# Kernel tuning notes

Hardware: AMD Instinct MI355X
Metric: run time of the kernel (lower is better)

Reference implementation:

```python
import jax, jax.numpy as jnp
import numpy as np

EMBED_DIM = 64
NUM_HEADS = 8
D_K = EMBED_DIM // NUM_HEADS  # 8
B, S = 8, 1024


def setup_inputs() -> dict:
    key = jax.random.key(0)
    ks = jax.random.split(key, 10)
    f32 = jnp.float32
    lim = 1.0 / np.sqrt(EMBED_DIM)
    def lin(k):
        kw, kb = jax.random.split(k)
        w = jax.random.uniform(kw, (EMBED_DIM, EMBED_DIM), f32, -lim, lim)
        b = jax.random.uniform(kb, (EMBED_DIM,), f32, -lim, lim)
        return w, b
    wq, bq = lin(ks[0])
    wk, bk = lin(ks[1])
    wv, bv = lin(ks[2])
    wo, bo = lin(ks[3])
    theta = jax.random.normal(ks[4], (EMBED_DIM,), f32)  # trainable RY angles, one per wire
    x = jax.random.normal(ks[5], (B, S, EMBED_DIM), f32)
    return {"x": x, "wq": wq, "bq": bq, "wk": wk, "bk": bk,
            "wv": wv, "bv": bv, "theta": theta, "wo": wo, "bo": bo}


def _quantum_map(t, theta):
    # Per-qubit circuit on |0>: RX(t_i) encode, RY(theta_i), <PauliZ_i>.
    # Product state => <Z_i> = cos(theta_i) * cos(t_i) exactly.
    return jnp.cos(theta) * jnp.cos(t.reshape(-1, EMBED_DIM))  # [N, E]


def reference(x, wq, bq, wk, bk, wv, bv, theta, wo, bo):
    # Linear QKV (torch nn.Linear: x @ W^T + b)
    q = x @ wq.T + bq
    k = x @ wk.T + bk
    v = x @ wv.T + bv
    # Quantum measurement map, flattened over batch*seq (as in the original)
    q_q = _quantum_map(q, theta)  # [N, E], N = B*S
    k_q = _quantum_map(k, theta)
    v_q = _quantum_map(v, theta)
    # Full flattened attention: [N, N] scores (original never reshapes back)
    scores = (q_q @ k_q.T) / jnp.sqrt(jnp.asarray(D_K, x.dtype))
    attn = jax.nn.softmax(scores, axis=-1)  # dropout is identity in eval
    out = attn @ v_q  # [N, E]
    return out @ wo.T + bo
```

## Files before the change

kernel.cpp:

```cpp
#include <hip/hip_runtime.h>
#include <hip/hip_bf16.h>

#define NQ 8192
#define DIM 64
#define SPLITS 16
#define FQB 64
#define KEYS_PER_SPLIT (NQ / SPLITS)
#define NSTEPS (KEYS_PER_SPLIT / 32)
#define GRID_FLASH ((NQ / FQB) * SPLITS)
#define MERGEB 1024
#define MROWS (NQ / MERGEB)
#define SC2 0.51012301920911057f
#define KSTR 72

typedef short s8v __attribute__((ext_vector_type(8)));
typedef short s4v __attribute__((ext_vector_type(4)));
typedef float f4v __attribute__((ext_vector_type(4)));
typedef int   i4v __attribute__((ext_vector_type(4)));

__device__ __forceinline__ float b2f(short s) {
  unsigned int u = ((unsigned int)(unsigned short)s) << 16;
  return __uint_as_float(u);
}
__device__ __forceinline__ float b2f_lo(unsigned int u) {
  return __uint_as_float(u << 16);
}
__device__ __forceinline__ float b2f_hi(unsigned int u) {
  return __uint_as_float(u & 0xffff0000u);
}
__device__ __forceinline__ short f2b(float f) {
  __hip_bfloat16 h = __float2bfloat16(f);
  return *reinterpret_cast<short*>(&h);
}
__device__ __forceinline__ int pack_bf16x2(float a, float b) {
  union { __hip_bfloat162 h; int i; } u;
  u.h = __float22bfloat162_rn(make_float2(a, b));
  return u.i;
}
__device__ __forceinline__ float fast_exp2(float x) {
#if __has_builtin(__builtin_amdgcn_exp2f)
  return __builtin_amdgcn_exp2f(x);
#else
  return exp2f(x);
#endif
}

__global__ __launch_bounds__(64) void qkv_kernel(
    const float* __restrict__ x,
    const float* __restrict__ wq, const float* __restrict__ bq,
    const float* __restrict__ wk, const float* __restrict__ bk,
    const float* __restrict__ wv, const float* __restrict__ bv,
    const float* __restrict__ theta,
    short* __restrict__ qq, short* __restrict__ kvT) {
  int lane = threadIdx.x & 63;
  int l15 = lane & 15, quad = lane >> 4;
  int tg = blockIdx.x;
  int mg = blockIdx.y;
  int n = tg * 16 + l15;

  const float* W  = (mg == 0) ? wq : (mg == 1) ? wk : wv;
  const float* Bb = (mg == 0) ? bq : (mg == 1) ? bk : bv;

  const float* xr = x + (size_t)n * DIM + quad * 8;
  float4 x0 = *(const float4*)&xr[0];
  float4 x1 = *(const float4*)&xr[4];
  float4 x2 = *(const float4*)&xr[32];
  float4 x3 = *(const float4*)&xr[36];
  s8v xf0 = {f2b(x0.x), f2b(x0.y), f2b(x0.z), f2b(x0.w),
             f2b(x1.x), f2b(x1.y), f2b(x1.z), f2b(x1.w)};
  s8v xf1 = {f2b(x2.x), f2b(x2.y), f2b(x2.z), f2b(x2.w),
             f2b(x3.x), f2b(x3.y), f2b(x3.z), f2b(x3.w)};

  size_t tb = (size_t)(n >> 6) * 8192;
  int nperm = (n & 3) | ((n & 16) >> 2);
  size_t vbase = tb + 4096 + ((n & 32) >> 5) * 2048 + ((n & 15) >> 2) * 128 + nperm;

#pragma unroll
  for (int i = 0; i < 4; ++i) {
    const float* wr = W + (size_t)(i * 16 + l15) * DIM + quad * 8;
    float4 a0 = *(const float4*)&wr[0];
    float4 a1 = *(const float4*)&wr[4];
    float4 a2 = *(const float4*)&wr[32];
    float4 a3 = *(const float4*)&wr[36];
    s8v wf0 = {f2b(a0.x), f2b(a0.y), f2b(a0.z), f2b(a0.w),
               f2b(a1.x), f2b(a1.y), f2b(a1.z), f2b(a1.w)};
    s8v wf1 = {f2b(a2.x), f2b(a2.y), f2b(a2.z), f2b(a2.w),
               f2b(a3.x), f2b(a3.y), f2b(a3.z), f2b(a3.w)};
    f4v acc = (f4v){0.f, 0.f, 0.f, 0.f};
    acc = __builtin_amdgcn_mfma_f32_16x16x32_bf16(wf0, xf0, acc, 0, 0, 0);
    acc = __builtin_amdgcn_mfma_f32_16x16x32_bf16(wf1, xf1, acc, 0, 0, 0);
    int d0 = i * 16 + quad * 4;
    float4 bias = *(const float4*)&Bb[d0];
    float4 th4 = *(const float4*)&theta[d0];
    float y0 = __cosf(acc[0] + bias.x) * __cosf(th4.x);
    float y1 = __cosf(acc[1] + bias.y) * __cosf(th4.y);
    float y2 = __cosf(acc[2] + bias.z) * __cosf(th4.z);
    float y3 = __cosf(acc[3] + bias.w) * __cosf(th4.w);
    if (mg == 0) {
      s4v p = {f2b(SC2 * y0), f2b(SC2 * y1), f2b(SC2 * y2), f2b(SC2 * y3)};
      *(s4v*)&qq[(size_t)n * DIM + d0] = p;
    } else if (mg == 1) {
      int e = d0;
      size_t idx = tb + ((n & 63) >> 4) * 1024 + (e >> 5) * 512 +
                   ((e & 31) >> 3) * 128 + (n & 15) * 8 + (e & 7);
      s4v p = {f2b(y0), f2b(y1), f2b(y2), f2b(y3)};
      *(s4v*)&kvT[idx] = p;
    } else {
      float ys[4] = {y0, y1, y2, y3};
#pragma unroll
      for (int r = 0; r < 4; ++r) {
        int e = d0 + r;
        kvT[vbase + (e >> 4) * 512 + (e & 15) * 8] = f2b(ys[r]);
      }
    }
  }
}

#if __has_builtin(__builtin_amdgcn_global_load_lds)
#define DMA_CHUNK(srcp, dstp) \
  __builtin_amdgcn_global_load_lds( \
      (const __attribute__((address_space(1))) void*)(srcp), \
      (__attribute__((address_space(3))) void*)(dstp), 16, 0, 0)
#else
#define DMA_CHUNK(srcp, dstp) \
  { *(s8v*)((short*)(dstp) + (threadIdx.x & 63) * 8) = \
        *(const s8v*)((const short*)(srcp)); }
#endif

__global__ __launch_bounds__(64, 2) void flash_kernel(
    const short* __restrict__ qq, const short* __restrict__ kvT,
    short* __restrict__ pO, short* __restrict__ pL) {
  __shared__ __align__(16) short lds[2][4096];

  int lane = threadIdx.x & 63;
  int l15 = lane & 15, quad = lane >> 4;
  int qblock = blockIdx.x >> 4, split = blockIdx.x & 15;
  int qbase = qblock * FQB;

  s8v qf[4][2];
#pragma unroll
  for (int qt = 0; qt < 4; ++qt) {
    const short* qr = qq + (qbase + qt * 16 + l15) * DIM + quad * 8;
    qf[qt][0] = *(const s8v*)qr;
    qf[qt][1] = *(const s8v*)(qr + 32);
  }
  asm volatile("s_waitcnt vmcnt(0)" ::: "memory");

  const short ONE = (short)0x3F80;
  const s8v ones = {ONE, ONE, ONE, ONE, ONE, ONE, ONE, ONE};

  f4v o[4][4], ol[4];
#pragma unroll
  for (int qt = 0; qt < 4; ++qt) {
    ol[qt] = (f4v){0.f, 0.f, 0.f, 0.f};
#pragma unroll
    for (int c = 0; c < 4; ++c) o[qt][c] = (f4v){0.f, 0.f, 0.f, 0.f};
  }

  const short* kvs = kvT + (size_t)(split * (KEYS_PER_SPLIT / 64)) * 8192 +
                     lane * 8;
#define STAGE32(S, BUF)                                                      \
  {                                                                          \
    const short* s_ = kvs + ((S) >> 1) * 8192 + ((S) & 1) * 2048;            \
    short* d_ = &lds[BUF][0];                                                \
    _Pragma("unroll") for (int c2 = 0; c2 < 4; ++c2) {                       \
      DMA_CHUNK(s_ + c2 * 512, d_ + c2 * 512);                               \
      DMA_CHUNK(s_ + 4096 + c2 * 512, d_ + 2048 + c2 * 512);                 \
    }                                                                        \
  }

  STAGE32(0, 0)

  for (int s = 0; s < NSTEPS; ++s) {
    if (s + 1 < NSTEPS) {
      STAGE32(s + 1, (s + 1) & 1)
      asm volatile("s_waitcnt vmcnt(8)" ::: "memory");
    } else {
      asm volatile("s_waitcnt vmcnt(0)" ::: "memory");
    }
    __builtin_amdgcn_sched_barrier(0);

    const short* kb = lds[s & 1];
    const short* vb = kb + 2048;

    i4v pai[4];
#pragma unroll
    for (int h = 0; h < 2; ++h) {
      s8v kf0 = *(const s8v*)&kb[(h * 2) * 512 + lane * 8];
      s8v kf1 = *(const s8v*)&kb[(h * 2 + 1) * 512 + lane * 8];
#pragma unroll
      for (int qt = 0; qt < 4; ++qt) {
        f4v acc = (f4v){0.f, 0.f, 0.f, 0.f};
        acc = __builtin_amdgcn_mfma_f32_16x16x32_bf16(kf0, qf[qt][0], acc, 0, 0, 0);
        acc = __builtin_amdgcn_mfma_f32_16x16x32_bf16(kf1, qf[qt][1], acc, 0, 0, 0);
        pai[qt][h * 2]     = pack_bf16x2(fast_exp2(acc[0]), fast_exp2(acc[1]));
        pai[qt][h * 2 + 1] = pack_bf16x2(fast_exp2(acc[2]), fast_exp2(acc[3]));
      }
    }
    __builtin_amdgcn_s_setprio(1);
#pragma unroll
    for (int qt = 0; qt < 4; ++qt)
      ol[qt] = __builtin_amdgcn_mfma_f32_16x16x32_bf16(
          __builtin_bit_cast(s8v, pai[qt]), ones, ol[qt], 0, 0, 0);
#pragma unroll
    for (int c = 0; c < 4; ++c) {
      s8v vf = *(const s8v*)&vb[c * 512 + lane * 8];
#pragma unroll
      for (int qt = 0; qt < 4; ++qt)
        o[qt][c] = __builtin_amdgcn_mfma_f32_16x16x32_bf16(
            __builtin_bit_cast(s8v, pai[qt]), vf, o[qt][c], 0, 0, 0);
    }
    __builtin_amdgcn_s_setprio(0);
  }

#pragma unroll
  for (int qt = 0; qt < 4; ++qt) {
#pragma unroll
    for (int r = 0; r < 4; ++r) {
      int q = qbase + qt * 16 + quad * 4 + r;
      short* dst = pO + ((size_t)split * NQ + q) * DIM;
#pragma unroll
      for (int c = 0; c < 4; ++c) dst[c * 16 + l15] = f2b(o[qt][c][r]);
      if (l15 == 0) pL[(size_t)split * NQ + q] = f2b(ol[qt][r]);
    }
  }
}

__global__ __launch_bounds__(256) void merge_kernel(
    const short* __restrict__ pO, const short* __restrict__ pL,
    const float* __restrict__ wo, const float* __restrict__ bo,
    float* __restrict__ out) {
  __shared__ __align__(16) short wsh[DIM * KSTR];
  __shared__ __align__(16) float att[MROWS * DIM];
  int tid = threadIdx.x;
  int q0 = blockIdx.x * MROWS;
  for (int i = tid; i < DIM * 16; i += 256) {
    int r = i >> 4, c4 = (i & 15) << 2;
    float4 w = *(const float4*)&wo[r * DIM + c4];
    s4v p = {f2b(w.x), f2b(w.y), f2b(w.z), f2b(w.w)};
    *(s4v*)&wsh[r * KSTR + c4] = p;
  }
  {
    int e2 = (tid & 31) * 2, rg8 = tid >> 5;
    int q = q0 + rg8;
    const short* psrc = pO + (size_t)q * DIM + e2;
    const short* lsrc = pL + q;
    float a0 = 0.f, a1 = 0.f, l = 0.f;
#pragma unroll
    for (int sp = 0; sp < SPLITS; ++sp) {
      unsigned int u = *(const unsigned int*)&psrc[(size_t)sp * NQ * DIM];
      a0 += b2f_lo(u);
      a1 += b2f_hi(u);
      l += b2f(lsrc[(size_t)sp * NQ]);
    }
#if __has_builtin(__builtin_amdgcn_rcpf)
    float ri = __builtin_amdgcn_rcpf(l);
#else
    float ri = 1.f / l;
#endif
    att[rg8 * DIM + e2] = a0 * ri;
    att[rg8 * DIM + e2 + 1] = a1 * ri;
  }
  __syncthreads();
  int e = tid & 63, rg = tid >> 6;
  for (int rr = rg; rr < MROWS; rr += 4) {
    float acc = bo[e];
#pragma unroll
    for (int c8 = 0; c8 < 8; ++c8) {
      s8v w = *(const s8v*)&wsh[e * KSTR + c8 * 8];
      const float* ar = &att[rr * DIM + c8 * 8];
      acc += ar[0] * b2f(w[0]) + ar[1] * b2f(w[1]) + ar[2] * b2f(w[2]) + ar[3] * b2f(w[3])
           + ar[4] * b2f(w[4]) + ar[5] * b2f(w[5]) + ar[6] * b2f(w[6]) + ar[7] * b2f(w[7]);
    }
    out[(size_t)(q0 + rr) * DIM + e] = acc;
  }
}

extern "C" void kernel_launch(void* const* d_in, const int* in_sizes, int n_in,
                              void* d_out, int out_size, void* d_ws, size_t ws_size,
                              hipStream_t stream) {
  const float* x  = (const float*)d_in[0];
  const float* wq = (const float*)d_in[1];
  const float* bq = (const float*)d_in[2];
  const float* wk = (const float*)d_in[3];
  const float* bk = (const float*)d_in[4];
  const float* wv = (const float*)d_in[5];
  const float* bv = (const float*)d_in[6];
  const float* th = (const float*)d_in[7];
  const float* wo = (const float*)d_in[8];
  const float* bo = (const float*)d_in[9];

  char* ws = (char*)d_ws;
  short* qq  = (short*)(ws);
  short* kvT = (short*)(ws + (1u << 20));
  short* pO  = (short*)(ws + (3u << 20));
  short* pL  = (short*)(ws + (19u << 20));

  hipLaunchKernelGGL(qkv_kernel, dim3(NQ / 16, 3), dim3(64), 0, stream,
                     x, wq, bq, wk, bk, wv, bv, th, qq, kvT);
  hipLaunchKernelGGL(flash_kernel, dim3(GRID_FLASH), dim3(FQB), 0, stream,
                     qq, kvT, pO, pL);
  hipLaunchKernelGGL(merge_kernel, dim3(MERGEB), dim3(256), 0, stream,
                     pO, pL, wo, bo, (float*)d_out);
}
```

Measured before the change: 113.6 us.

## Fuse split merge and output projection into flash kernel via last-block atomic counter

Removes the separate merge kernel. Each flash block atomically increments a per-query-block counter, and the last split to finish reduces the partial outputs and row sums, then applies the output projection with bf16 MFMA. The counters are zeroed by qkv_kernel. This saves a kernel launch and the merge kernel's separate pass, but puts a serial tail of merge work on the last-arriving blocks and adds fences and atomics. LDS per block also grows.

```diff
diff --git a/kernel.cpp b/kernel.cpp
--- a/kernel.cpp
+++ b/kernel.cpp
@@ -8,10 +8,9 @@
 #define KEYS_PER_SPLIT (NQ / SPLITS)
 #define NSTEPS (KEYS_PER_SPLIT / 32)
 #define GRID_FLASH ((NQ / FQB) * SPLITS)
-#define MERGEB 1024
-#define MROWS (NQ / MERGEB)
+#define NQB (NQ / FQB)
 #define SC2 0.51012301920911057f
-#define KSTR 72
+#define ATTSTR 68
 
 typedef short s8v __attribute__((ext_vector_type(8)));
 typedef short s4v __attribute__((ext_vector_type(4)));
@@ -44,6 +43,13 @@
   return exp2f(x);
 #endif
 }
+__device__ __forceinline__ float fast_rcp(float x) {
+#if __has_builtin(__builtin_amdgcn_rcpf)
+  return __builtin_amdgcn_rcpf(x);
+#else
+  return 1.f / x;
+#endif
+}
 
 __global__ __launch_bounds__(64) void qkv_kernel(
     const float* __restrict__ x,
@@ -51,12 +57,17 @@
     const float* __restrict__ wk, const float* __restrict__ bk,
     const float* __restrict__ wv, const float* __restrict__ bv,
     const float* __restrict__ theta,
-    short* __restrict__ qq, short* __restrict__ kvT) {
+    short* __restrict__ qq, short* __restrict__ kvT, int* __restrict__ cnt) {
   int lane = threadIdx.x & 63;
   int l15 = lane & 15, quad = lane >> 4;
   int tg = blockIdx.x;
   int mg = blockIdx.y;
   int n = tg * 16 + l15;
+
+  if ((tg | mg) == 0) {
+    cnt[lane] = 0;
+    cnt[lane + 64] = 0;
+  }
 
   const float* W  = (mg == 0) ? wq : (mg == 1) ? wk : wv;
   const float* Bb = (mg == 0) ? bq : (mg == 1) ? bk : bv;
@@ -129,8 +140,11 @@
 
 __global__ __launch_bounds__(64, 2) void flash_kernel(
     const short* __restrict__ qq, const short* __restrict__ kvT,
-    short* __restrict__ pO, short* __restrict__ pL) {
-  __shared__ __align__(16) short lds[2][4096];
+    short* __restrict__ pO, short* __restrict__ pL,
+    const float* __restrict__ wo, const float* __restrict__ bo,
+    float* __restrict__ out, int* __restrict__ cnt) {
+  __shared__ __align__(16) char smem[17664];
+  short* stage = (short*)smem;
 
   int lane = threadIdx.x & 63;
   int l15 = lane & 15, quad = lane >> 4;
@@ -162,7 +176,7 @@
 #define STAGE32(S, BUF)                                                      \
   {                                                                          \
     const short* s_ = kvs + ((S) >> 1) * 8192 + ((S) & 1) * 2048;            \
-    short* d_ = &lds[BUF][0];                                                \
+    short* d_ = stage + (BUF) * 4096;                                        \
     _Pragma("unroll") for (int c2 = 0; c2 < 4; ++c2) {                       \
       DMA_CHUNK(s_ + c2 * 512, d_ + c2 * 512);                               \
       DMA_CHUNK(s_ + 4096 + c2 * 512, d_ + 2048 + c2 * 512);                 \
@@ -180,7 +194,7 @@
     }
     __builtin_amdgcn_sched_barrier(0);
 
-    const short* kb = lds[s & 1];
+    const short* kb = stage + (s & 1) * 4096;
     const short* vb = kb + 2048;
 
     i4v pai[4];
@@ -224,55 +238,78 @@
       if (l15 == 0) pL[(size_t)split * NQ + q] = f2b(ol[qt][r]);
     }
   }
-}
-
-__global__ __launch_bounds__(256) void merge_kernel(
-    const short* __restrict__ pO, const short* __restrict__ pL,
-    const float* __restrict__ wo, const float* __restrict__ bo,
-    float* __restrict__ out) {
-  __shared__ __align__(16) short wsh[DIM * KSTR];
-  __shared__ __align__(16) float att[MROWS * DIM];
-  int tid = threadIdx.x;
-  int q0 = blockIdx.x * MROWS;
-  for (int i = tid; i < DIM * 16; i += 256) {
-    int r = i >> 4, c4 = (i & 15) << 2;
-    float4 w = *(const float4*)&wo[r * DIM + c4];
-    s4v p = {f2b(w.x), f2b(w.y), f2b(w.z), f2b(w.w)};
-    *(s4v*)&wsh[r * KSTR + c4] = p;
-  }
+
+  __threadfence();
+  int old = 0;
+  if (lane == 0) old = atomicAdd(&cnt[qblock], 1);
+  old = __shfl(old, 0);
+  if (old != SPLITS - 1) return;
+  __threadfence();
+
+  float* attf = (float*)smem;
+  float* rif  = attf + 64 * ATTSTR;
+
   {
-    int e2 = (tid & 31) * 2, rg8 = tid >> 5;
-    int q = q0 + rg8;
-    const short* psrc = pO + (size_t)q * DIM + e2;
-    const short* lsrc = pL + q;
-    float a0 = 0.f, a1 = 0.f, l = 0.f;
-#pragma unroll
-    for (int sp = 0; sp < SPLITS; ++sp) {
-      unsigned int u = *(const unsigned int*)&psrc[(size_t)sp * NQ * DIM];
-      a0 += b2f_lo(u);
-      a1 += b2f_hi(u);
-      l += b2f(lsrc[(size_t)sp * NQ]);
-    }
-#if __has_builtin(__builtin_amdgcn_rcpf)
-    float ri = __builtin_amdgcn_rcpf(l);
-#else
-    float ri = 1.f / l;
-#endif
-    att[rg8 * DIM + e2] = a0 * ri;
-    att[rg8 * DIM + e2 + 1] = a1 * ri;
-  }
-  __syncthreads();
-  int e = tid & 63, rg = tid >> 6;
-  for (int rr = rg; rr < MROWS; rr += 4) {
-    float acc = bo[e];
-#pragma unroll
-    for (int c8 = 0; c8 < 8; ++c8) {
-      s8v w = *(const s8v*)&wsh[e * KSTR + c8 * 8];
-      const float* ar = &att[rr * DIM + c8 * 8];
-      acc += ar[0] * b2f(w[0]) + ar[1] * b2f(w[1]) + ar[2] * b2f(w[2]) + ar[3] * b2f(w[3])
-           + ar[4] * b2f(w[4]) + ar[5] * b2f(w[5]) + ar[6] * b2f(w[6]) + ar[7] * b2f(w[7]);
-    }
-    out[(size_t)(q0 + rr) * DIM + e] = acc;
+    const short* lp = pL + qbase + lane;
+    float lsum = 0.f;
+#pragma unroll
+    for (int sp = 0; sp < SPLITS; ++sp) lsum += b2f(lp[(size_t)sp * NQ]);
+    rif[lane] = fast_rcp(lsum);
+  }
+  {
+    int e2 = lane & 31, half = lane >> 5;
+    const short* psrc = pO + ((size_t)(qbase + half)) * DIM + e2 * 2;
+#pragma unroll 4
+    for (int r2 = 0; r2 < 32; ++r2) {
+      int row = r2 * 2 + half;
+      const short* pr = psrc + (size_t)r2 * 2 * DIM;
+      float a0 = 0.f, a1 = 0.f;
+#pragma unroll
+      for (int sp = 0; sp < SPLITS; ++sp) {
+        unsigned int u = *(const unsigned int*)&pr[(size_t)sp * NQ * DIM];
+        a0 += b2f_lo(u);
+        a1 += b2f_hi(u);
+      }
+      *(float2*)&attf[row * ATTSTR + e2 * 2] = make_float2(a0, a1);
+    }
+  }
+
+  s8v bf[4][2];
+  float bov[4];
+#pragma unroll
+  for (int ct = 0; ct < 4; ++ct) {
+    const float* wr = wo + (size_t)(ct * 16 + l15) * DIM + quad * 8;
+    float4 c0 = *(const float4*)&wr[0];
+    float4 c1 = *(const float4*)&wr[4];
+    float4 c2 = *(const float4*)&wr[32];
+    float4 c3 = *(const float4*)&wr[36];
+    bf[ct][0] = {f2b(c0.x), f2b(c0.y), f2b(c0.z), f2b(c0.w),
+                 f2b(c1.x), f2b(c1.y), f2b(c1.z), f2b(c1.w)};
+    bf[ct][1] = {f2b(c2.x), f2b(c2.y), f2b(c2.z), f2b(c2.w),
+                 f2b(c3.x), f2b(c3.y), f2b(c3.z), f2b(c3.w)};
+    bov[ct] = bo[ct * 16 + l15];
+  }
+#pragma unroll
+  for (int rt = 0; rt < 4; ++rt) {
+    int row = rt * 16 + l15;
+    float riv = rif[row];
+    const float* ar = &attf[row * ATTSTR + quad * 8];
+    s8v af0 = {f2b(ar[0] * riv), f2b(ar[1] * riv), f2b(ar[2] * riv),
+               f2b(ar[3] * riv), f2b(ar[4] * riv), f2b(ar[5] * riv),
+               f2b(ar[6] * riv), f2b(ar[7] * riv)};
+    s8v af1 = {f2b(ar[32] * riv), f2b(ar[33] * riv), f2b(ar[34] * riv),
+               f2b(ar[35] * riv), f2b(ar[36] * riv), f2b(ar[37] * riv),
+               f2b(ar[38] * riv), f2b(ar[39] * riv)};
+#pragma unroll
+    for (int ct = 0; ct < 4; ++ct) {
+      f4v acc = (f4v){0.f, 0.f, 0.f, 0.f};
+      acc = __builtin_amdgcn_mfma_f32_16x16x32_bf16(af0, bf[ct][0], acc, 0, 0, 0);
+      acc = __builtin_amdgcn_mfma_f32_16x16x32_bf16(af1, bf[ct][1], acc, 0, 0, 0);
+#pragma unroll
+      for (int r = 0; r < 4; ++r)
+        out[(size_t)(qbase + rt * 16 + quad * 4 + r) * DIM + ct * 16 + l15] =
+            acc[r] + bov[ct];
+    }
   }
 }
 
@@ -295,11 +332,10 @@
   short* kvT = (short*)(ws + (1u << 20));
   short* pO  = (short*)(ws + (3u << 20));
   short* pL  = (short*)(ws + (19u << 20));
+  int*   cnt = (int*)(ws + (19u << 20) + (256u << 10));
 
   hipLaunchKernelGGL(qkv_kernel, dim3(NQ / 16, 3), dim3(64), 0, stream,
-                     x, wq, bq, wk, bk, wv, bv, th, qq, kvT);
+                     x, wq, bq, wk, bk, wv, bv, th, qq, kvT, cnt);
   hipLaunchKernelGGL(flash_kernel, dim3(GRID_FLASH), dim3(FQB), 0, stream,
-                     qq, kvT, pO, pL);
-  hipLaunchKernelGGL(merge_kernel, dim3(MERGEB), dim3(256), 0, stream,
-                     pO, pL, wo, bo, (float*)d_out);
-}
+                     qq, kvT, pO, pL, wo, bo, (float*)d_out, cnt);
+}
```

New measurement: 269.1 us. 2.37x slower.
